# Kernel tuning notes

Hardware: AMD Instinct MI355X
Metric: run time of the kernel (lower is better)

The kernel has to match this reference:

```python
import jax, jax.numpy as jnp
import numpy as np
from jax import lax

B, C, H, W = 2, 192, 256, 256
HEADS = 6
QC = 4 * C  # elementwise gate: q, gate, k, v
EPS = 1e-12


def setup_inputs() -> dict:
    key = jax.random.key(0)
    ks = jax.random.split(key, 8)
    x = jax.random.normal(ks[0], (B, C, H, W), dtype=jnp.float32)
    qkv_w = jax.random.normal(ks[1], (QC, C), dtype=jnp.float32) * (1.0 / np.sqrt(C))
    qkv_b = jax.random.normal(ks[2], (QC,), dtype=jnp.float32) * 0.02
    dw_w = jax.random.normal(ks[3], (QC, 1, 3, 3), dtype=jnp.float32) * (1.0 / 3.0)
    dw_b = jax.random.normal(ks[4], (QC,), dtype=jnp.float32) * 0.02
    temperature = jnp.ones((HEADS, 1, 1), dtype=jnp.float32)
    proj_w = jax.random.normal(ks[5], (C, C), dtype=jnp.float32) * (1.0 / np.sqrt(C))
    proj_b = jax.random.normal(ks[6], (C,), dtype=jnp.float32) * 0.02
    return {"x": x, "qkv_w": qkv_w, "qkv_b": qkv_b, "dw_w": dw_w, "dw_b": dw_b,
            "temperature": temperature, "proj_w": proj_w, "proj_b": proj_b}


def reference(x, qkv_w, qkv_b, dw_w, dw_b, temperature, proj_w, proj_b):
    b, c, h, w = x.shape
    hd = c // HEADS  # head_dim
    n = h * w
    # 1x1 conv qkv projection
    qkv = jnp.einsum('bchw,oc->bohw', x, qkv_w) + qkv_b[None, :, None, None]
    # 3x3 depthwise conv (groups == channels)
    qkv = lax.conv_general_dilated(
        qkv, dw_w, window_strides=(1, 1), padding=((1, 1), (1, 1)),
        dimension_numbers=('NCHW', 'OIHW', 'NCHW'), feature_group_count=QC)
    qkv = qkv + dw_b[None, :, None, None]
    # split: q, gate (elementwise), k, v
    q = qkv[:, :c]
    gate = qkv[:, c:2 * c]
    k = qkv[:, 2 * c:3 * c]
    v = qkv[:, 3 * c:]
    # b (head c) h w -> b head c (h w)
    def to_heads(t):
        return t.reshape(b, HEADS, hd, n)
    q, k, v, gate = to_heads(q), to_heads(k), to_heads(v), to_heads(gate)
    # L2 normalize along token dim (matches F.normalize eps clamp)
    q = q / jnp.maximum(jnp.sqrt(jnp.sum(q * q, axis=-1, keepdims=True)), EPS)
    k = k / jnp.maximum(jnp.sqrt(jnp.sum(k * k, axis=-1, keepdims=True)), EPS)
    # channel attention: [b, head, hd, hd]
    attn = jnp.einsum('bhcn,bhdn->bhcd', q, k) * temperature[None]
    attn = jax.nn.softmax(attn, axis=-1)
    out = jnp.einsum('bhcd,bhdn->bhcn', attn, v)
    out = out * jax.nn.sigmoid(gate)
    out = out.reshape(b, c, h, w)
    out = jnp.einsum('bchw,oc->bohw', out, proj_w) + proj_b[None, :, None, None]
    return out
```

## Files before the change

kernel.cpp:

```cpp
#include <hip/hip_runtime.h>
#include <math.h>


#define HEADS 6
#define CDIM 192
#define QCH 768
#define HH 256
#define WW 256
#define NPIX 65536
#define PADC 200
#define GNT 4

typedef __bf16 bf16x8 __attribute__((ext_vector_type(8)));
typedef float f32x4 __attribute__((ext_vector_type(4)));
typedef unsigned short u16x8 __attribute__((ext_vector_type(8)));

__device__ __forceinline__ float b2f(unsigned short u) {
  union { unsigned int i; float f; } x; x.i = ((unsigned int)u) << 16; return x.f;
}
__device__ __forceinline__ unsigned short f2b(float f) {
  union { float f; unsigned int i; } x; x.f = f;
  unsigned int lsb = (x.i >> 16) & 1u;
  x.i += 0x7fffu + lsb;
  return (unsigned short)(x.i >> 16);
}

__global__ void zero_init(float* __restrict__ p, int n) {
  int i = blockIdx.x * 256 + threadIdx.x;
  if (i < n) p[i] = 0.f;
}

__global__ __launch_bounds__(256)
void w2bf(const float* __restrict__ qkv_w, const float* __restrict__ proj_w,
          unsigned short* __restrict__ wbf) {
  int id = blockIdx.x * 256 + threadIdx.x;
  if (id >= 5 * 192 * 192) return;
  int k = id % 192;
  int m = (id / 192) % 192;
  int q = id / (192 * 192);
  float v = (q < 4) ? qkv_w[(size_t)(q * 192 + m) * 192 + k]
                    : proj_w[(size_t)m * 192 + k];
  wbf[((size_t)q * 192 + m) * PADC + k] = f2b(v);
}

__global__ __launch_bounds__(256)
void x2t(const float* __restrict__ x, unsigned short* __restrict__ xT) {
  __shared__ unsigned short tile[64 * PADC];
  int t = threadIdx.x;
  int n0 = blockIdx.x * 64;
  int b = blockIdx.y;
  #pragma unroll
  for (int i = 0; i < 12; ++i) {
    int idx = t + i * 256;
    int c = idx >> 4;
    int nn4 = (idx & 15) << 2;
    float4 v = *(const float4*)(x + ((size_t)b * CDIM + c) * NPIX + n0 + nn4);
    tile[(nn4 + 0) * PADC + c] = f2b(v.x);
    tile[(nn4 + 1) * PADC + c] = f2b(v.y);
    tile[(nn4 + 2) * PADC + c] = f2b(v.z);
    tile[(nn4 + 3) * PADC + c] = f2b(v.w);
  }
  __syncthreads();
  #pragma unroll
  for (int i = 0; i < 6; ++i) {
    int idx = t + i * 256;
    int row = idx / 24;
    int c8 = (idx % 24) * 8;
    *(u16x8*)(xT + ((size_t)b * NPIX + n0 + row) * PADC + c8) =
        *(const u16x8*)(tile + row * PADC + c8);
  }
}

__global__ __launch_bounds__(256)
void gemm_t(const unsigned short* __restrict__ wq0,
            const unsigned short* __restrict__ wq1,
            const float* __restrict__ bias0,
            const float* __restrict__ bias1,
            const unsigned short* __restrict__ Bsrc,
            unsigned short* __restrict__ outB)
{
  __shared__ unsigned short b_lds[64 * PADC];
  int t = threadIdx.x;
  int mt = blockIdx.y;
  int half = mt / 3;
  int mrow = (mt % 3) * 64;
  int b = blockIdx.z;
  int wid = t >> 6, lane = t & 63;
  int r = lane & 15, quad = lane >> 4;

  const unsigned short* wq = (half ? wq1 : wq0) + (size_t)mrow * PADC;
  bf16x8 wreg[4][6];
  #pragma unroll
  for (int nt = 0; nt < 4; ++nt) {
    #pragma unroll
    for (int k6 = 0; k6 < 6; ++k6)
      wreg[nt][k6] = *(const bf16x8*)(wq + (size_t)(nt * 16 + r) * PADC + k6 * 32 + quad * 8);
  }
  const float* bp = half ? bias1 : bias0;
  float bb[4];
  #pragma unroll
  for (int nt = 0; nt < 4; ++nt) bb[nt] = bp[mrow + nt * 16 + r];

  unsigned short* op = outB + (size_t)(b * 2 + half) * CDIM * NPIX;

  for (int ni = 0; ni < GNT; ++ni) {
    int n0 = (blockIdx.x * GNT + ni) * 64;
    const unsigned short* Bs = Bsrc + ((size_t)b * NPIX + n0) * PADC;
    #pragma unroll
    for (int i = 0; i < 6; ++i) {
      int idx = t + i * 256;
      *(u16x8*)(b_lds + idx * 8) = *(const u16x8*)(Bs + (size_t)idx * 8);
    }
    if (t < 64) {
      int idx = 1536 + t;
      *(u16x8*)(b_lds + idx * 8) = *(const u16x8*)(Bs + (size_t)idx * 8);
    }
    __syncthreads();

    f32x4 acc[4];
    #pragma unroll
    for (int nt = 0; nt < 4; ++nt) acc[nt] = (f32x4){0.f, 0.f, 0.f, 0.f};

    #pragma unroll
    for (int k6 = 0; k6 < 6; ++k6) {
      bf16x8 xf = *(const bf16x8*)(b_lds + (wid * 16 + r) * PADC + k6 * 32 + quad * 8);
      #pragma unroll
      for (int nt = 0; nt < 4; ++nt)
        acc[nt] = __builtin_amdgcn_mfma_f32_16x16x32_bf16(xf, wreg[nt][k6], acc[nt], 0, 0, 0);
    }

    size_t n = (size_t)n0 + wid * 16 + quad * 4;
    #pragma unroll
    for (int nt = 0; nt < 4; ++nt) {
      int m = mrow + nt * 16 + r;
      ushort4 uu;
      uu.x = f2b(acc[nt][0] + bb[nt]); uu.y = f2b(acc[nt][1] + bb[nt]);
      uu.z = f2b(acc[nt][2] + bb[nt]); uu.w = f2b(acc[nt][3] + bb[nt]);
      *(ushort4*)(op + (size_t)m * NPIX + n) = uu;
    }
    __syncthreads();
  }
}

__global__ __launch_bounds__(256)
void proj_fused(const unsigned short* __restrict__ wproj,
                const float* __restrict__ bias,
                const unsigned short* __restrict__ post2,
                const unsigned short* __restrict__ Pbf,
                float* __restrict__ out)
{
  __shared__ unsigned short a_lds[64 * PADC];
  __shared__ unsigned short b_lds[64 * PADC];
  int t = threadIdx.x;
  int n0 = blockIdx.x * 64;
  int b = blockIdx.y;
  int wid = t >> 6, lane = t & 63;
  int r = lane & 15, quad = lane >> 4;
  int nl = wid * 16 + r;
  size_t n = (size_t)n0 + nl;

  const unsigned short* vbase = post2 + (size_t)(b * 2 + 0) * CDIM * NPIX;
  const unsigned short* gbase = post2 + (size_t)(b * 2 + 1) * CDIM * NPIX;
  const unsigned short* Pb = Pbf + (size_t)b * HEADS * 1024;

  #pragma unroll
  for (int h = 0; h < HEADS; ++h) {
    union { unsigned short u[8]; bf16x8 v; } vf;
    #pragma unroll
    for (int j = 0; j < 8; ++j)
      vf.u[j] = vbase[(size_t)(h * 32 + quad * 8 + j) * NPIX + n];
    #pragma unroll
    for (int c0 = 0; c0 < 32; c0 += 16) {
      bf16x8 pf = *(const bf16x8*)(Pb + h * 1024 + (c0 + r) * 32 + quad * 8);
      f32x4 d = (f32x4){0.f, 0.f, 0.f, 0.f};
      d = __builtin_amdgcn_mfma_f32_16x16x32_bf16(pf, vf.v, d, 0, 0, 0);
      #pragma unroll
      for (int i = 0; i < 4; ++i) {
        int c = c0 + quad * 4 + i;
        float gg = b2f(gbase[(size_t)(h * 32 + c) * NPIX + n]);
        float sg = 1.f / (1.f + __expf(-gg));
        b_lds[nl * PADC + h * 32 + c] = f2b(d[i] * sg);
      }
    }
  }

  #pragma unroll
  for (int mt = 0; mt < 3; ++mt) {
    int mrow = mt * 64;
    const unsigned short* wq = wproj + (size_t)mrow * PADC;

    __syncthreads();
    #pragma unroll
    for (int i = 0; i < 6; ++i) {
      int idx = t + i * 256;
      *(u16x8*)(a_lds + idx * 8) = *(const u16x8*)(wq + (size_t)idx * 8);
    }
    if (t < 64) {
      int idx = 1536 + t;
      *(u16x8*)(a_lds + idx * 8) = *(const u16x8*)(wq + (size_t)idx * 8);
    }
    __syncthreads();

    f32x4 acc[4];
    #pragma unroll
    for (int nt = 0; nt < 4; ++nt) acc[nt] = (f32x4){0.f, 0.f, 0.f, 0.f};

    #pragma unroll
    for (int kk = 0; kk < 192; kk += 32) {
      bf16x8 xf = *(const bf16x8*)(b_lds + (wid * 16 + r) * PADC + kk + quad * 8);
      #pragma unroll
      for (int nt = 0; nt < 4; ++nt) {
        bf16x8 wf = *(const bf16x8*)(a_lds + (nt * 16 + r) * PADC + kk + quad * 8);
        acc[nt] = __builtin_amdgcn_mfma_f32_16x16x32_bf16(xf, wf, acc[nt], 0, 0, 0);
      }
    }

    size_t nn = (size_t)n0 + wid * 16 + quad * 4;
    float* op = out + (size_t)b * CDIM * NPIX;
    #pragma unroll
    for (int nt = 0; nt < 4; ++nt) {
      int m = mrow + nt * 16 + r;
      float bbv = bias[m];
      float4 vv;
      vv.x = acc[nt][0] + bbv; vv.y = acc[nt][1] + bbv;
      vv.z = acc[nt][2] + bbv; vv.w = acc[nt][3] + bbv;
      *(float4*)(op + (size_t)m * NPIX + nn) = vv;
    }
  }
}

__global__ __launch_bounds__(256)
void dwconv_ssq(const unsigned short* __restrict__ in,
                const float* __restrict__ w9,
                const float* __restrict__ bias,
                unsigned short* __restrict__ outp,
                float* __restrict__ ssqBase,
                int qs0, int qs1)
{
  __shared__ unsigned short lds[34][256];
  __shared__ float red[4];
  int t = threadIdx.x;
  int z = blockIdx.z;
  int qsel = (z & 1) ? qs1 : qs0;
  int o  = blockIdx.x >> 3;
  int ry = blockIdx.x & 7;
  int y0 = ry << 5;

  const unsigned short* base = in + ((size_t)z * CDIM + o) * NPIX;
  #pragma unroll
  for (int i = 0; i < 9; ++i) {
    int idx = t + i * 256;
    if (idx < 2176) {
      int row = idx >> 6;
      int c4  = (idx & 63) << 2;
      int gy  = y0 - 1 + row;
      ushort4 vv = make_ushort4(0, 0, 0, 0);
      if (gy >= 0 && gy < HH)
        vv = *(const ushort4*)(base + (size_t)gy * WW + c4);
      *(ushort4*)(&lds[row][c4]) = vv;
    }
  }

  float wv[9];
  #pragma unroll
  for (int i = 0; i < 9; ++i) wv[i] = w9[((size_t)qsel * CDIM + o) * 9 + i];
  float bo = bias[qsel * CDIM + o];
  __syncthreads();

  int w = t >> 6, lane = t & 63;
  int x0 = lane << 2;
  float sumsq = 0.f;
  unsigned short* outbase = outp + ((size_t)z * CDIM + o) * NPIX;

  #pragma unroll
  for (int i = 0; i < 8; ++i) {
    int yo = w * 8 + i;
    float a0 = bo, a1 = bo, a2 = bo, a3 = bo;
    #pragma unroll
    for (int dy = 0; dy < 3; ++dy) {
      ushort4 mv = *(const ushort4*)(&lds[yo + dy][x0]);
      float v0 = b2f(mv.x), v1 = b2f(mv.y), v2 = b2f(mv.z), v3 = b2f(mv.w);
      float vl = __shfl_up(v3, 1, 64);   if (lane == 0)  vl = 0.f;
      float vr = __shfl_down(v0, 1, 64); if (lane == 63) vr = 0.f;
      float w0 = wv[dy * 3 + 0], w1 = wv[dy * 3 + 1], w2 = wv[dy * 3 + 2];
      a0 += w0 * vl + w1 * v0 + w2 * v1;
      a1 += w0 * v0 + w1 * v1 + w2 * v2;
      a2 += w0 * v1 + w1 * v2 + w2 * v3;
      a3 += w0 * v2 + w1 * v3 + w2 * vr;
    }
    ushort4 ov;
    ov.x = f2b(a0); ov.y = f2b(a1); ov.z = f2b(a2); ov.w = f2b(a3);
    *(ushort4*)(outbase + (size_t)(y0 + yo) * WW + x0) = ov;
    if (ssqBase != nullptr) sumsq += a0 * a0 + a1 * a1 + a2 * a2 + a3 * a3;
  }

  if (ssqBase != nullptr) {
    float* ssq = ssqBase + (size_t)(z >> 1) * 2 * CDIM + (z & 1) * CDIM;
    #pragma unroll
    for (int off = 32; off; off >>= 1) sumsq += __shfl_down(sumsq, off, 64);
    if (lane == 0) red[w] = sumsq;
    __syncthreads();
    if (t == 0) atomicAdd(&ssq[o], red[0] + red[1] + red[2] + red[3]);
  }
}

__global__ __launch_bounds__(256)
void gram(const unsigned short* __restrict__ post,
          float* __restrict__ S)
{
  int h = blockIdx.y, b = blockIdx.z;
  int t = threadIdx.x, wid = t >> 6, lane = t & 63;
  int r = lane & 15, quad = lane >> 4;
  int c0 = (wid >> 1) * 16, d0 = (wid & 1) * 16;
  size_t nb = (size_t)blockIdx.x * 512 + quad * 8;
  const unsigned short* qrow =
      post + ((size_t)(b * 2 + 0) * CDIM + h * 32 + c0 + r) * NPIX + nb;
  const unsigned short* krow =
      post + ((size_t)(b * 2 + 1) * CDIM + h * 32 + d0 + r) * NPIX + nb;
  f32x4 acc = (f32x4){0.f, 0.f, 0.f, 0.f};
  #pragma unroll
  for (int kk = 0; kk < 512; kk += 32) {
    bf16x8 af  = *(const bf16x8*)(qrow + kk);
    bf16x8 bfr = *(const bf16x8*)(krow + kk);
    acc = __builtin_amdgcn_mfma_f32_16x16x32_bf16(af, bfr, acc, 0, 0, 0);
  }
  float* Sp = S + ((size_t)b * HEADS + h) * 1024;
  #pragma unroll
  for (int i = 0; i < 4; ++i)
    atomicAdd(&Sp[(c0 + quad * 4 + i) * 32 + (d0 + r)], acc[i]);
}

__global__ void softmax_scale(const float* __restrict__ S,
                              const float* __restrict__ ssq,
                              const float* __restrict__ temp,
                              unsigned short* __restrict__ Pbf)
{
  int h = blockIdx.x, b = blockIdx.y;
  int t = threadIdx.x;
  int c = t >> 5, d = t & 31;
  float nq = fmaxf(sqrtf(ssq[(size_t)b * 2 * CDIM + h * 32 + c]), 1e-12f);
  float nk = fmaxf(sqrtf(ssq[(size_t)b * 2 * CDIM + CDIM + h * 32 + d]), 1e-12f);
  float v = S[((size_t)b * HEADS + h) * 1024 + t] / (nq * nk) * temp[h];
  float m = v;
  for (int off = 16; off; off >>= 1) m = fmaxf(m, __shfl_xor(m, off, 32));
  float e = expf(v - m);
  float s = e;
  for (int off = 16; off; off >>= 1) s += __shfl_xor(s, off, 32);
  Pbf[((size_t)b * HEADS + h) * 1024 + c * 32 + d] = f2b(e / s);
}

extern "C" void kernel_launch(void* const* d_in, const int* in_sizes, int n_in,
                              void* d_out, int out_size, void* d_ws, size_t ws_size,
                              hipStream_t stream)
{
  const float* x      = (const float*)d_in[0];
  const float* qkv_w  = (const float*)d_in[1];
  const float* qkv_b  = (const float*)d_in[2];
  const float* dw_w   = (const float*)d_in[3];
  const float* dw_b   = (const float*)d_in[4];
  const float* temp   = (const float*)d_in[5];
  const float* proj_w = (const float*)d_in[6];
  const float* proj_b = (const float*)d_in[7];
  float* out = (float*)d_out;

  char* ws = (char*)d_ws;
  const size_t qbytes  = (size_t)CDIM * NPIX * 2;
  const size_t xTbytes = (size_t)2 * NPIX * PADC * 2;
  const size_t wbytes  = (size_t)5 * 192 * PADC * 2;
  unsigned short* xT    = (unsigned short*)ws;
  unsigned short* wbf   = (unsigned short*)(ws + xTbytes);
  unsigned short* pre   = (unsigned short*)(ws + xTbytes + wbytes);
  unsigned short* post  = (unsigned short*)(ws + xTbytes + wbytes + 4 * qbytes);
  unsigned short* post2 = (unsigned short*)(ws + xTbytes + wbytes + 8 * qbytes);
  float* S   = (float*)(ws + xTbytes + wbytes + 12 * qbytes);
  float* ssq = S + 2 * HEADS * 1024;
  unsigned short* Pbf = (unsigned short*)(ssq + 2 * 2 * CDIM);
  const int nz = 2 * HEADS * 1024 + 2 * 2 * CDIM;

  zero_init<<<(nz + 255) / 256, 256, 0, stream>>>(S, nz);
  w2bf<<<(5 * 192 * 192 + 255) / 256, 256, 0, stream>>>(qkv_w, proj_w, wbf);
  x2t<<<dim3(NPIX / 64, 2), 256, 0, stream>>>(x, xT);

  const unsigned short* wq = wbf;
  const size_t wqs = (size_t)192 * PADC;

  gemm_t<<<dim3(NPIX / (64 * GNT), 6, 2), 256, 0, stream>>>(
      wq + 0 * wqs, wq + 2 * wqs, qkv_b + 0 * CDIM, qkv_b + 2 * CDIM, xT, pre);
  dwconv_ssq<<<dim3(CDIM * 8, 1, 4), 256, 0, stream>>>(pre, dw_w, dw_b, post, ssq, 0, 2);

  gemm_t<<<dim3(NPIX / (64 * GNT), 6, 2), 256, 0, stream>>>(
      wq + 3 * wqs, wq + 1 * wqs, qkv_b + 3 * CDIM, qkv_b + 1 * CDIM, xT, pre);
  dwconv_ssq<<<dim3(CDIM * 8, 1, 4), 256, 0, stream>>>(pre, dw_w, dw_b, post2, nullptr, 3, 1);

  gram<<<dim3(128, HEADS, 2), 256, 0, stream>>>(post, S);
  softmax_scale<<<dim3(HEADS, 2), 1024, 0, stream>>>(S, ssq, temp, Pbf);

  proj_fused<<<dim3(NPIX / 64, 2), 256, 0, stream>>>(
      wq + 4 * wqs, proj_b, post2, Pbf, out);
}
```

Before: 512.4 us.

## Stage v/gate tiles through LDS in proj and prefetch qkv GEMM tiles in registers

In the projection kernel, v and gate tiles are now loaded with coalesced 16-byte global reads into padded LDS buffers, replacing strided per-element global gathers. The gated attention outputs are held in registers and written to the B tile only after a barrier, so the LDS space can be aliased. In the qkv GEMM, the next input tile is prefetched into registers while MFMAs run on the current one, and GNT doubles so each block handles more tiles. This adds register pressure and larger LDS use, which may lower occupancy.

```diff
diff --git a/kernel.cpp b/kernel.cpp
--- a/kernel.cpp
+++ b/kernel.cpp
@@ -9,11 +9,12 @@
 #define WW 256
 #define NPIX 65536
 #define PADC 200
-#define GNT 4
+#define GNT 8
 
 typedef __bf16 bf16x8 __attribute__((ext_vector_type(8)));
 typedef float f32x4 __attribute__((ext_vector_type(4)));
 typedef unsigned short u16x8 __attribute__((ext_vector_type(8)));
+typedef unsigned short u16x4 __attribute__((ext_vector_type(4)));
 
 __device__ __forceinline__ float b2f(unsigned short u) {
   union { unsigned int i; float f; } x; x.i = ((unsigned int)u) << 16; return x.f;
@@ -103,19 +104,30 @@
 
   unsigned short* op = outB + (size_t)(b * 2 + half) * CDIM * NPIX;
 
+  u16x8 st[6]; u16x8 st7;
+  {
+    const unsigned short* Bs = Bsrc + ((size_t)b * NPIX + (size_t)blockIdx.x * GNT * 64) * PADC;
+    #pragma unroll
+    for (int i = 0; i < 6; ++i)
+      st[i] = *(const u16x8*)(Bs + (size_t)(t + i * 256) * 8);
+    if (t < 64) st7 = *(const u16x8*)(Bs + (size_t)(1536 + t) * 8);
+  }
+
   for (int ni = 0; ni < GNT; ++ni) {
-    int n0 = (blockIdx.x * GNT + ni) * 64;
-    const unsigned short* Bs = Bsrc + ((size_t)b * NPIX + n0) * PADC;
-    #pragma unroll
-    for (int i = 0; i < 6; ++i) {
-      int idx = t + i * 256;
-      *(u16x8*)(b_lds + idx * 8) = *(const u16x8*)(Bs + (size_t)idx * 8);
-    }
-    if (t < 64) {
-      int idx = 1536 + t;
-      *(u16x8*)(b_lds + idx * 8) = *(const u16x8*)(Bs + (size_t)idx * 8);
-    }
+    #pragma unroll
+    for (int i = 0; i < 6; ++i)
+      *(u16x8*)(b_lds + (t + i * 256) * 8) = st[i];
+    if (t < 64) *(u16x8*)(b_lds + (1536 + t) * 8) = st7;
     __syncthreads();
+
+    if (ni + 1 < GNT) {
+      const unsigned short* Bs =
+          Bsrc + ((size_t)b * NPIX + ((size_t)blockIdx.x * GNT + ni + 1) * 64) * PADC;
+      #pragma unroll
+      for (int i = 0; i < 6; ++i)
+        st[i] = *(const u16x8*)(Bs + (size_t)(t + i * 256) * 8);
+      if (t < 64) st7 = *(const u16x8*)(Bs + (size_t)(1536 + t) * 8);
+    }
 
     f32x4 acc[4];
     #pragma unroll
@@ -129,6 +141,7 @@
         acc[nt] = __builtin_amdgcn_mfma_f32_16x16x32_bf16(xf, wreg[nt][k6], acc[nt], 0, 0, 0);
     }
 
+    int n0 = ((int)blockIdx.x * GNT + ni) * 64;
     size_t n = (size_t)n0 + wid * 16 + quad * 4;
     #pragma unroll
     for (int nt = 0; nt < 4; ++nt) {
@@ -149,38 +162,68 @@
                 const unsigned short* __restrict__ Pbf,
                 float* __restrict__ out)
 {
-  __shared__ unsigned short a_lds[64 * PADC];
-  __shared__ unsigned short b_lds[64 * PADC];
+  __shared__ unsigned char smem[52224];
+  unsigned short* v_lds = (unsigned short*)smem;
+  unsigned short* g_lds = (unsigned short*)(smem + 26112);
+  unsigned short* b_l   = (unsigned short*)smem;
+  unsigned short* a_l   = (unsigned short*)(smem + 25600);
+
   int t = threadIdx.x;
   int n0 = blockIdx.x * 64;
   int b = blockIdx.y;
   int wid = t >> 6, lane = t & 63;
   int r = lane & 15, quad = lane >> 4;
   int nl = wid * 16 + r;
-  size_t n = (size_t)n0 + nl;
 
   const unsigned short* vbase = post2 + (size_t)(b * 2 + 0) * CDIM * NPIX;
   const unsigned short* gbase = post2 + (size_t)(b * 2 + 1) * CDIM * NPIX;
   const unsigned short* Pb = Pbf + (size_t)b * HEADS * 1024;
 
   #pragma unroll
+  for (int i = 0; i < 6; ++i) {
+    int idx = t + i * 256;
+    int row = idx >> 3, sub = idx & 7;
+    u16x8 vv = *(const u16x8*)(vbase + (size_t)row * NPIX + n0 + sub * 8);
+    u16x8 gg = *(const u16x8*)(gbase + (size_t)row * NPIX + n0 + sub * 8);
+    unsigned short* vd = v_lds + row * 68 + sub * 8;
+    unsigned short* gd = g_lds + row * 68 + sub * 8;
+    *(u16x4*)(vd)     = (u16x4){vv[0], vv[1], vv[2], vv[3]};
+    *(u16x4*)(vd + 4) = (u16x4){vv[4], vv[5], vv[6], vv[7]};
+    *(u16x4*)(gd)     = (u16x4){gg[0], gg[1], gg[2], gg[3]};
+    *(u16x4*)(gd + 4) = (u16x4){gg[4], gg[5], gg[6], gg[7]};
+  }
+  __syncthreads();
+
+  float attr[HEADS][8];
+  #pragma unroll
   for (int h = 0; h < HEADS; ++h) {
     union { unsigned short u[8]; bf16x8 v; } vf;
     #pragma unroll
     for (int j = 0; j < 8; ++j)
-      vf.u[j] = vbase[(size_t)(h * 32 + quad * 8 + j) * NPIX + n];
-    #pragma unroll
-    for (int c0 = 0; c0 < 32; c0 += 16) {
+      vf.u[j] = v_lds[(h * 32 + quad * 8 + j) * 68 + nl];
+    #pragma unroll
+    for (int c8 = 0; c8 < 2; ++c8) {
+      int c0 = c8 * 16;
       bf16x8 pf = *(const bf16x8*)(Pb + h * 1024 + (c0 + r) * 32 + quad * 8);
       f32x4 d = (f32x4){0.f, 0.f, 0.f, 0.f};
       d = __builtin_amdgcn_mfma_f32_16x16x32_bf16(pf, vf.v, d, 0, 0, 0);
       #pragma unroll
       for (int i = 0; i < 4; ++i) {
         int c = c0 + quad * 4 + i;
-        float gg = b2f(gbase[(size_t)(h * 32 + c) * NPIX + n]);
-        float sg = 1.f / (1.f + __expf(-gg));
-        b_lds[nl * PADC + h * 32 + c] = f2b(d[i] * sg);
+        float gg = b2f(g_lds[(h * 32 + c) * 68 + nl]);
+        attr[h][c8 * 4 + i] = d[i] / (1.f + __expf(-gg));
       }
+    }
+  }
+  __syncthreads();
+
+  #pragma unroll
+  for (int h = 0; h < HEADS; ++h) {
+    #pragma unroll
+    for (int c8 = 0; c8 < 2; ++c8) {
+      #pragma unroll
+      for (int i = 0; i < 4; ++i)
+        b_l[nl * PADC + h * 32 + c8 * 16 + quad * 4 + i] = f2b(attr[h][c8 * 4 + i]);
     }
   }
 
@@ -193,11 +236,11 @@
     #pragma unroll
     for (int i = 0; i < 6; ++i) {
       int idx = t + i * 256;
-      *(u16x8*)(a_lds + idx * 8) = *(const u16x8*)(wq + (size_t)idx * 8);
+      *(u16x8*)(a_l + idx * 8) = *(const u16x8*)(wq + (size_t)idx * 8);
     }
     if (t < 64) {
       int idx = 1536 + t;
-      *(u16x8*)(a_lds + idx * 8) = *(const u16x8*)(wq + (size_t)idx * 8);
+      *(u16x8*)(a_l + idx * 8) = *(const u16x8*)(wq + (size_t)idx * 8);
     }
     __syncthreads();
 
@@ -207,10 +250,10 @@
 
     #pragma unroll
     for (int kk = 0; kk < 192; kk += 32) {
-      bf16x8 xf = *(const bf16x8*)(b_lds + (wid * 16 + r) * PADC + kk + quad * 8);
+      bf16x8 xf = *(const bf16x8*)(b_l + (wid * 16 + r) * PADC + kk + quad * 8);
       #pragma unroll
       for (int nt = 0; nt < 4; ++nt) {
-        bf16x8 wf = *(const bf16x8*)(a_lds + (nt * 16 + r) * PADC + kk + quad * 8);
+        bf16x8 wf = *(const bf16x8*)(a_l + (nt * 16 + r) * PADC + kk + quad * 8);
         acc[nt] = __builtin_amdgcn_mfma_f32_16x16x32_bf16(xf, wf, acc[nt], 0, 0, 0);
       }
     }
```

Result: faster. 484.2 us (-5.5%).
